# Performance work log

Measured on AMD Instinct MI355X. Metric: run time of the kernel, lower is better.

Reference implementation:

```python
import jax, jax.numpy as jnp
import numpy as np

TOPK = 16
MIN_SIM = 0.05
MIN_VOTES = 0.3
REMOVE_INNER = 0.5
NUM_CLASSES = 1000


def setup_inputs() -> dict:
    key = jax.random.key(0)
    kq, kdb, kid, kxy, kwh = jax.random.split(key, 5)
    Qn, N, C = 1024, 200000, 256
    q = jax.random.normal(kq, (Qn, C), dtype=jnp.float32)
    q = q / jnp.linalg.norm(q, axis=1, keepdims=True)
    db = jax.random.normal(kdb, (N, C), dtype=jnp.float32)
    db = db / jnp.linalg.norm(db, axis=1, keepdims=True)
    ids = jax.random.randint(kid, (N,), 0, NUM_CLASSES).astype(jnp.float32)
    places_db = jnp.concatenate([db, ids[:, None]], axis=1)  # (N, C+1)
    xy = jax.random.uniform(kxy, (Qn, 2), minval=0.0, maxval=800.0)
    wh = jax.random.uniform(kwh, (Qn, 2), minval=10.0, maxval=200.0)
    boxes = jnp.concatenate([xy, xy + wh], axis=1)  # valid xyxy boxes
    return {"boxes": boxes, "descriptors": q, "places_db": places_db}


def _remove_overlapping_boxes(boxes, labels, thr):
    # overlap = intersection / min(area_i, area_j); drop the BIGGER box of any
    # same-label pair whose overlap >= thr.
    bf = boxes.astype(jnp.float32)
    x1, y1, x2, y2 = bf[:, 0], bf[:, 1], bf[:, 2], bf[:, 3]
    areas = (x2 - x1) * (y2 - y1)
    xi1 = jnp.maximum(x1[:, None], x1[None, :])
    yi1 = jnp.maximum(y1[:, None], y1[None, :])
    xi2 = jnp.minimum(x2[:, None], x2[None, :])
    yi2 = jnp.minimum(y2[:, None], y2[None, :])
    inter = jnp.clip(xi2 - xi1, 0.0) * jnp.clip(yi2 - yi1, 0.0)
    area_i, area_j = areas[:, None], areas[None, :]
    area_small = jnp.minimum(area_i, area_j)
    overlap = jnp.where(area_small > 0, inter / jnp.maximum(area_small, 1e-12), 0.0)
    same_lbl = (labels[:, None] == labels[None, :]) & (labels[:, None] >= 0)
    n = boxes.shape[0]
    non_diag = ~jnp.eye(n, dtype=bool)
    mask_pair = same_lbl & (overlap >= thr) & non_diag
    bigger_i = area_i > area_j
    remove_i = (mask_pair & bigger_i).any(axis=1)
    remove_j = (mask_pair & ~bigger_i).any(axis=0)
    remove = remove_i | remove_j
    return jnp.where(remove, jnp.full_like(labels, -1), labels)


def reference(boxes, descriptors, places_db):
    X = places_db[:, :-1]                       # (N, C)
    ids = places_db[:, -1].astype(jnp.int32)    # (N,)
    sims = descriptors @ X.T                    # (Q, N)
    top_sims, top_idx = jax.lax.top_k(sims, TOPK)   # (Q, topk)
    top_ids = ids[top_idx]                          # (Q, topk)
    mask_sim = top_sims >= MIN_SIM
    # one-hot majority vote over classes
    one_hot = (top_ids[:, :, None] == jnp.arange(NUM_CLASSES, dtype=jnp.int32)[None, None, :]).astype(jnp.float32)
    vote_counts = (one_hot * mask_sim[:, :, None].astype(jnp.float32)).sum(axis=1)  # (Q, NUM_CLASSES)
    majority_counts = vote_counts.max(axis=1)
    majority_ids = jnp.argmax(vote_counts, axis=1).astype(jnp.int32)
    valid_votes = mask_sim.sum(axis=1).astype(jnp.float32)
    vote_ratio = jnp.where(valid_votes > 0, majority_counts / jnp.maximum(valid_votes, 1.0), 0.0)
    valid = (majority_counts > 0) & (vote_ratio >= MIN_VOTES)
    results = jnp.where(valid, majority_ids, jnp.full_like(majority_ids, -1))
    results = _remove_overlapping_boxes(boxes, results, REMOVE_INNER)
    match = (top_ids == results[:, None]) & mask_sim
    sim_scores = jnp.where(match, top_sims, jnp.zeros_like(top_sims)).max(axis=1)
    valid_mask = (results >= 0) & jnp.isfinite(sim_scores) & jnp.isfinite(boxes).all(axis=1)
    # Static-shape variant of the original's compaction: invalid rows are
    # marked with class=-1 / score=0 instead of being sliced out.
    return (boxes,
            jnp.where(valid_mask, sim_scores, 0.0),
            jnp.where(valid_mask, results, -1))
```

## Files before the change

kernel.cpp:

```cpp
#include <hip/hip_runtime.h>
#include <hip/hip_bf16.h>

#define QN 1024
#define NDB 200000
#define NDB_PAD 200064
#define PDBW 257
#define CDIM 256
#define TK 16
#define NEGF (-1e30f)
#define MIN_SIM_C 0.05f
#define MIN_VOTES_C 0.3f

#define NCH 256
#define THETA 0.19f
#define CAPQ 10
#define NCHUNK1 49
#define CPQ1 (NCHUNK1*32)

typedef __attribute__((ext_vector_type(8))) short bf16x8;
typedef __attribute__((ext_vector_type(4))) float f32x4;
typedef __attribute__((ext_vector_type(8))) int   i32x8;
typedef __attribute__((ext_vector_type(4))) int   i32x4;

__device__ __forceinline__ short f2bf(float f) {
  union { float f; unsigned u; } x; x.f = f;
  unsigned u = x.u;
  return (short)((u + 0x7fffu + ((u >> 16) & 1u)) >> 16);
}

__device__ __forceinline__ void async_copy16(const void* gp, void* lp) {
  __builtin_amdgcn_global_load_lds(
      (__attribute__((address_space(1))) void*)gp,
      (__attribute__((address_space(3))) void*)lp, 16, 0, 0);
}

__device__ __forceinline__ unsigned pk_fp8x4(float a, float b, float c, float d) {
  unsigned w = (unsigned)__builtin_amdgcn_cvt_pk_fp8_f32(a, b, 0, false);
  w = (unsigned)__builtin_amdgcn_cvt_pk_fp8_f32(c, d, (int)w, true);
  return w;
}

__device__ __forceinline__ int chunk_nsub(int c) { return 12 + (c < 54 ? 1 : 0); }
__device__ __forceinline__ int chunk_row0(int c) { return (12*c + (c < 54 ? c : 54)) << 6; }

__global__ __launch_bounds__(256) void convert_db_kernel(
    const float* __restrict__ pdb, unsigned char* __restrict__ dbb,
    int* __restrict__ flag)
{
  if (blockIdx.x == 0 && threadIdx.x == 0) *flag = 0;
  const int wv = (int)threadIdx.x >> 6, lane = (int)threadIdx.x & 63;
  for (int r = (int)blockIdx.x*4 + wv; r < NDB_PAD; r += (int)gridDim.x*4) {
    unsigned pack = 0u;
    if (r < NDB) {
      const float* p = pdb + (size_t)r*PDBW + lane*4;
      pack = pk_fp8x4(p[0], p[1], p[2], p[3]);
    }
    const int piece = lane >> 1;
    const int ps    = piece ^ ((r & 15) << 1);
    *(unsigned*)(dbb + (size_t)r*256 + ps*8 + (lane & 1)*4) = pack;
  }
}

__global__ __launch_bounds__(512, 1) void sims_filter_kernel(
    const float* __restrict__ qd, const unsigned char* __restrict__ dbb,
    unsigned int* __restrict__ seg_g, unsigned int* __restrict__ cnt_g)
{
  __shared__ __align__(16) char db_lds[2][64 * 256];
  __shared__ unsigned seg_lds[8][64][CAPQ];
  __shared__ int lcnt[8][64];

  const int tid  = (int)threadIdx.x;
  const int lane = tid & 63;
  const int wv   = tid >> 6;
  const int cid  = (int)blockIdx.x;
  const int mt   = (int)blockIdx.y;
  const int nsub = chunk_nsub(cid);
  const int row0 = chunk_row0(cid);

  lcnt[wv][lane] = 0;

  const int l15  = lane & 15;
  const int egrp = lane >> 4;
  const int rowb = egrp << 2;
  const int colb = l15;

  i32x8 aq[4][2];
  {
    #pragma unroll
    for (int fm = 0; fm < 4; ++fm) {
      const float* qrow = qd + (size_t)(mt*512 + wv*64 + fm*16 + l15)*CDIM;
      #pragma unroll
      for (int kk = 0; kk < 2; ++kk) {
        const float* p = qrow + kk*128 + egrp*32;
        i32x8 a;
        #pragma unroll
        for (int d = 0; d < 8; ++d) {
          float4 x = *(const float4*)(p + d*4);
          a[d] = (int)pk_fp8x4(x.x, x.y, x.z, x.w);
        }
        aq[fm][kk] = a;
      }
    }
  }

  const char* dbbase = (const char*)dbb;
#define STAGE(bufi, tile) do { \
    const char* _src = dbbase + ((size_t)(row0 + (tile)*64) * 256) + wv*2048 + lane*16; \
    char* _dst = (char*)db_lds[(bufi)] + wv*2048 + lane*16; \
    async_copy16(_src,        _dst); \
    async_copy16(_src + 1024, _dst + 1024); \
  } while (0)

  STAGE(0, 0);

  for (int s = 0; s < nsub; ++s) {
    asm volatile("s_waitcnt vmcnt(0)" ::: "memory");
    __builtin_amdgcn_sched_barrier(0);
    __builtin_amdgcn_s_barrier();
    __builtin_amdgcn_sched_barrier(0);

    if (s + 1 < nsub) STAGE((s + 1) & 1, s + 1);

    const char* dbt = (const char*)db_lds[s & 1];
    #pragma unroll
    for (int h = 0; h < 2; ++h) {
      f32x4 acc[4][2];
      #pragma unroll
      for (int fm = 0; fm < 4; ++fm)
        #pragma unroll
        for (int fnl = 0; fnl < 2; ++fnl)
          acc[fm][fnl] = (f32x4){0.f, 0.f, 0.f, 0.f};

      __builtin_amdgcn_s_setprio(1);
      #pragma unroll
      for (int kk = 0; kk < 2; ++kk) {
        #pragma unroll
        for (int fnl = 0; fnl < 2; ++fnl) {
          const int fn = h*2 + fnl;
          const char* rowp = dbt + (fn*16 + l15)*256;
          const int mbase = kk*8 + egrp*2;
          i32x4 lo = *(const i32x4*)(rowp + (((mbase    ) ^ l15) << 4));
          i32x4 hi = *(const i32x4*)(rowp + (((mbase + 1) ^ l15) << 4));
          i32x8 b = __builtin_shufflevector(lo, hi, 0, 1, 2, 3, 4, 5, 6, 7);
          #pragma unroll
          for (int fm = 0; fm < 4; ++fm)
            acc[fm][fnl] = __builtin_amdgcn_mfma_scale_f32_16x16x128_f8f6f4(
                aq[fm][kk], b, acc[fm][fnl],
                0 , 0 ,
                0, 0x7F7F7F7Fu , 0, 0x7F7F7F7Fu );
        }
      }
      __builtin_amdgcn_s_setprio(0);

      #pragma unroll
      for (int fm = 0; fm < 4; ++fm)
        #pragma unroll
        for (int fnl = 0; fnl < 2; ++fnl) {
          const f32x4 a = acc[fm][fnl];
          const float m = fmaxf(fmaxf(a[0], a[1]), fmaxf(a[2], a[3]));
          if (m > THETA) {
            #pragma unroll
            for (int j = 0; j < 4; ++j) {
              if (a[j] > THETA) {
                const int ql = fm*16 + rowb + j;
                const int slot = atomicAdd(&lcnt[wv][ql], 1);
                if (slot < CAPQ) {
                  const unsigned v16 = (unsigned)(unsigned short)f2bf(a[j]);
                  const unsigned loc = (unsigned)(s*64 + (h*2 + fnl)*16 + colb);
                  seg_lds[wv][ql][slot] = (v16 << 16) | loc;
                }
              }
            }
          }
        }
    }

    asm volatile("s_waitcnt lgkmcnt(0)" ::: "memory");
    __builtin_amdgcn_sched_barrier(0);
  }
#undef STAGE

  {
    const int cnt = lcnt[wv][lane];
    const int qg = mt*512 + wv*64 + lane;
    cnt_g[qg*NCH + cid] = (unsigned)cnt;
    const int nc = min(cnt, CAPQ);
    unsigned* dst = seg_g + (size_t)(qg*NCH + cid)*CAPQ;
    for (int j = 0; j < nc; ++j) dst[j] = seg_lds[wv][lane][j];
  }
}

__global__ __launch_bounds__(64) void gather_vote_kernel(
    const float* __restrict__ pdb,
    const unsigned* __restrict__ seg_g, const unsigned* __restrict__ cnt_g,
    int* __restrict__ out_label, float* __restrict__ out_s, int* __restrict__ flag)
{
  __shared__ float    cv[NCH*CAPQ];
  __shared__ unsigned ci[NCH*CAPQ];
  const int q    = (int)blockIdx.x;
  const int lane = (int)threadIdx.x;

  bool over = false;
  int tot = 0;
  #pragma unroll
  for (int h = 0; h < NCH/64; ++h) {
    const int c = h*64 + lane;
    const int cnt = (int)cnt_g[q*NCH + c];
    over |= (cnt > CAPQ);
    const int nc = min(cnt, CAPQ);
    tot += nc;
    const int r0c = chunk_row0(c);
    const unsigned* src = seg_g + (size_t)(q*NCH + c)*CAPQ;
    for (int j = 0; j < CAPQ; ++j) {
      float v = NEGF; unsigned idx = 0u;
      if (j < nc) {
        const unsigned e = src[j];
        v = __uint_as_float(e & 0xFFFF0000u);
        idx = (unsigned)(r0c + (int)(e & 0xFFFFu));
      }
      cv[c*CAPQ + j] = v;
      ci[c*CAPQ + j] = idx;
    }
  }
  #pragma unroll
  for (int off = 32; off >= 1; off >>= 1) tot += __shfl_xor(tot, off);
  __syncthreads();

  float topv[TK]; int topid[TK];
  #pragma unroll
  for (int r = 0; r < TK; ++r) {
    float bv = NEGF; int bp = -1;
    #pragma unroll 4
    for (int j = 0; j < (NCH*CAPQ)/64; ++j) {
      const int p = j*64 + lane;
      const float v = cv[p];
      if (v > bv) { bv = v; bp = p; }
    }
    #pragma unroll
    for (int off = 32; off >= 1; off >>= 1) {
      const float ov = __shfl_xor(bv, off);
      const int   op = __shfl_xor(bp, off);
      if (ov > bv || (ov == bv && ((unsigned)op < (unsigned)bp))) { bv = ov; bp = op; }
    }
    topv[r] = bv;
    int id = -2;
    if (bp >= 0 && bv > NEGF) id = (int)pdb[(size_t)ci[bp]*PDBW + CDIM];
    topid[r] = id;
    if (lane == 0 && bp >= 0) cv[bp] = NEGF;
    __syncthreads();
  }

  if (lane == 0) {
    bool mk[TK];
    int nvalid = 0;
    #pragma unroll
    for (int i = 0; i < TK; ++i) {
      mk[i] = (topv[i] >= MIN_SIM_C) && (topid[i] >= 0);
      nvalid += mk[i] ? 1 : 0;
    }
    int maj = 0, majid = 0x7fffffff;
    for (int i = 0; i < TK; ++i) {
      if (!mk[i]) continue;
      int c = 0;
      for (int j = 0; j < TK; ++j) c += (mk[j] && topid[j] == topid[i]) ? 1 : 0;
      if (c > maj || (c == maj && topid[i] < majid)) { maj = c; majid = topid[i]; }
    }
    const float ratio = (float)maj / fmaxf((float)nvalid, 1.0f);
    const bool valid = (maj > 0) && (ratio >= MIN_VOTES_C);
    const int label = valid ? majid : -1;
    float s = 0.f;
    #pragma unroll
    for (int i = 0; i < TK; ++i)
      if (mk[i] && topid[i] == label) s = fmaxf(s, topv[i]);
    out_label[q] = label;
    out_s[q]     = s;
  }
  const bool bad = (__ballot(over) != 0ull) || (tot < TK);
  if (lane == 0 && bad) atomicOr(flag, 1);
}

__global__ __launch_bounds__(256, 2) void sims_topk1_kernel(
    const float* __restrict__ qd, const float* __restrict__ pdb,
    float* __restrict__ cand_val, unsigned int* __restrict__ cand_idx,
    const int* __restrict__ gate)
{
  if (gate && *gate == 0) return;
  __shared__ __align__(16) short db_lds[128 * 264];
  float* sims = (float*)db_lds;

  const int tid  = (int)threadIdx.x;
  const int lane = tid & 63;
  const int wv   = tid >> 6;
  const int cid   = (int)blockIdx.x;
  const int mtile = (int)blockIdx.y;

  bf16x8 aq[2][8];
  {
    const int l15 = lane & 15;
    const int kb  = (lane >> 4) << 3;
    #pragma unroll
    for (int fm = 0; fm < 2; ++fm) {
      const int row = mtile*128 + wv*32 + fm*16 + l15;
      #pragma unroll
      for (int kk = 0; kk < 8; ++kk) {
        const float* p = qd + (size_t)row*CDIM + kk*32 + kb;
        float4 x0 = *(const float4*)p;
        float4 x1 = *(const float4*)(p + 4);
        bf16x8 a;
        a[0]=f2bf(x0.x); a[1]=f2bf(x0.y); a[2]=f2bf(x0.z); a[3]=f2bf(x0.w);
        a[4]=f2bf(x1.x); a[5]=f2bf(x1.y); a[6]=f2bf(x1.z); a[7]=f2bf(x1.w);
        aq[fm][kk] = a;
      }
    }
  }

  float    tv[TK];
  unsigned ti[TK];
  #pragma unroll
  for (int i = 0; i < TK; ++i) { tv[i] = NEGF; ti[i] = 0u; }
  float minv = NEGF; int minp = 0;

  const int g0chunk = cid * 4096;
  const int q_l  = tid & 127;
  const int half = tid >> 7;

  for (int s = 0; s < 32; ++s) {
    const int g0 = g0chunk + s*128;
    {
      const int rb = tid >> 6;
      const int c4 = (tid & 63) << 2;
      for (int i = 0; i < 32; ++i) {
        const int rl = i*4 + rb;
        const int g  = g0 + rl;
        float v0, v1, v2, v3;
        if (g < NDB) {
          const float* p = pdb + (size_t)g*PDBW + c4;
          v0 = p[0]; v1 = p[1]; v2 = p[2]; v3 = p[3];
        } else { v0 = v1 = v2 = v3 = 0.f; }
        short* d = &db_lds[rl*264 + c4];
        d[0]=f2bf(v0); d[1]=f2bf(v1); d[2]=f2bf(v2); d[3]=f2bf(v3);
      }
    }
    __syncthreads();

    f32x4 acc[2][8];
    #pragma unroll
    for (int fm = 0; fm < 2; ++fm)
      #pragma unroll
      for (int fn = 0; fn < 8; ++fn)
        acc[fm][fn] = (f32x4){0.f, 0.f, 0.f, 0.f};
    {
      const int l15 = lane & 15;
      const int kb  = (lane >> 4) << 3;
      #pragma unroll
      for (int kk = 0; kk < 8; ++kk) {
        bf16x8 b[8];
        #pragma unroll
        for (int fn = 0; fn < 8; ++fn)
          b[fn] = *(const bf16x8*)&db_lds[(fn*16 + l15)*264 + kk*32 + kb];
        #pragma unroll
        for (int fn = 0; fn < 8; ++fn) {
          acc[0][fn] = __builtin_amdgcn_mfma_f32_16x16x32_bf16(aq[0][kk], b[fn], acc[0][fn], 0, 0, 0);
          acc[1][fn] = __builtin_amdgcn_mfma_f32_16x16x32_bf16(aq[1][kk], b[fn], acc[1][fn], 0, 0, 0);
        }
      }
    }
    __syncthreads();

    {
      const int colb = lane & 15;
      const int rowb = (lane >> 4) << 2;
      #pragma unroll
      for (int fm = 0; fm < 2; ++fm)
        #pragma unroll
        for (int fn = 0; fn < 8; ++fn)
          #pragma unroll
          for (int j = 0; j < 4; ++j)
            sims[(wv*32 + fm*16 + rowb + j)*129 + fn*16 + colb] = acc[fm][fn][j];
    }
    __syncthreads();

    {
      const int cb = half * 64;
      #pragma unroll 4
      for (int c = 0; c < 64; ++c) {
        const int colc = cb + c;
        const float v = sims[q_l*129 + colc];
        const int g = g0 + colc;
        if (v > minv && g < NDB) {
          #pragma unroll
          for (int i = 0; i < TK; ++i) if (i == minp) { tv[i] = v; ti[i] = (unsigned)g; }
          minv = tv[0]; minp = 0;
          #pragma unroll
          for (int i = 1; i < TK; ++i) if (tv[i] < minv) { minv = tv[i]; minp = i; }
        }
      }
    }
    __syncthreads();
  }

  {
    const int qg = mtile*128 + q_l;
    float*    pv = cand_val + ((size_t)qg*NCHUNK1 + cid)*32 + half*TK;
    unsigned* pi = cand_idx + ((size_t)qg*NCHUNK1 + cid)*32 + half*TK;
    #pragma unroll
    for (int i = 0; i < TK; ++i) { pv[i] = tv[i]; pi[i] = ti[i]; }
  }
}

template<int CPQ>
__global__ __launch_bounds__(64) void merge_vote_kernel(
    const float* __restrict__ pdb,
    const float* __restrict__ cand_val, const unsigned* __restrict__ cand_idx,
    int* __restrict__ out_label, float* __restrict__ out_s,
    const int* __restrict__ gate)
{
  if (gate && *gate == 0) return;
  __shared__ float    cv[CPQ];
  __shared__ unsigned ci[CPQ];
  const int q    = (int)blockIdx.x;
  const int lane = (int)threadIdx.x;

  for (int j = lane; j < CPQ; j += 64) {
    cv[j] = cand_val[(size_t)q*CPQ + j];
    ci[j] = cand_idx[(size_t)q*CPQ + j];
  }
  __syncthreads();

  float topv[TK]; int topid[TK];
  #pragma unroll
  for (int r = 0; r < TK; ++r) {
    float bv = NEGF; int bp = -1;
    for (int j = lane; j < CPQ; j += 64) {
      const float v = cv[j];
      if (v > bv) { bv = v; bp = j; }
    }
    #pragma unroll
    for (int off = 32; off >= 1; off >>= 1) {
      const float ov = __shfl_xor(bv, off);
      const int   op = __shfl_xor(bp, off);
      if (ov > bv || (ov == bv && ((unsigned)op < (unsigned)bp))) { bv = ov; bp = op; }
    }
    topv[r] = bv;
    int id = -2;
    if (bp >= 0 && bv > NEGF) id = (int)pdb[(size_t)ci[bp]*PDBW + CDIM];
    topid[r] = id;
    if (lane == 0 && bp >= 0) cv[bp] = NEGF;
    __syncthreads();
  }

  if (lane == 0) {
    bool mk[TK];
    int nvalid = 0;
    #pragma unroll
    for (int i = 0; i < TK; ++i) {
      mk[i] = (topv[i] >= MIN_SIM_C) && (topid[i] >= 0);
      nvalid += mk[i] ? 1 : 0;
    }
    int maj = 0, majid = 0x7fffffff;
    for (int i = 0; i < TK; ++i) {
      if (!mk[i]) continue;
      int c = 0;
      for (int j = 0; j < TK; ++j) c += (mk[j] && topid[j] == topid[i]) ? 1 : 0;
      if (c > maj || (c == maj && topid[i] < majid)) { maj = c; majid = topid[i]; }
    }
    const float ratio = (float)maj / fmaxf((float)nvalid, 1.0f);
    const bool valid = (maj > 0) && (ratio >= MIN_VOTES_C);
    const int label = valid ? majid : -1;
    float s = 0.f;
    #pragma unroll
    for (int i = 0; i < TK; ++i)
      if (mk[i] && topid[i] == label) s = fmaxf(s, topv[i]);
    out_label[q] = label;
    out_s[q]     = s;
  }
}

__device__ __forceinline__ bool finitef(float v) {
  return ((__float_as_uint(v) >> 23) & 0xffu) != 0xffu;
}

__global__ __launch_bounds__(64) void finalize_kernel(
    const float* __restrict__ boxes, const int* __restrict__ labels,
    const float* __restrict__ svals, float* __restrict__ out)
{
  const int x    = (int)blockIdx.x;
  const int lane = (int)threadIdx.x;
  const int lx = labels[x];
  const float bx1 = boxes[x*4+0], by1 = boxes[x*4+1];
  const float bx2 = boxes[x*4+2], by2 = boxes[x*4+3];
  const float ax = (bx2 - bx1) * (by2 - by1);

  bool flag = false;
  if (lx >= 0) {
    for (int y = lane; y < QN; y += 64) {
      if (y == x) continue;
      if (labels[y] != lx) continue;
      const float c1 = boxes[y*4+0], c2 = boxes[y*4+1];
      const float c3 = boxes[y*4+2], c4 = boxes[y*4+3];
      const float ay = (c3 - c1) * (c4 - c2);
      const float xi1 = fmaxf(bx1, c1), yi1 = fmaxf(by1, c2);
      const float xi2 = fminf(bx2, c3), yi2 = fminf(by2, c4);
      const float inter = fmaxf(xi2 - xi1, 0.f) * fmaxf(yi2 - yi1, 0.f);
      const float asmall = fminf(ax, ay);
      const float ov = (asmall > 0.f) ? inter / fmaxf(asmall, 1e-12f) : 0.f;
      if (ov >= 0.5f && ay <= ax) flag = true;
    }
  }
  const bool removed = (__ballot(flag) != 0ull);
  const int label = removed ? -1 : lx;
  const float s = svals[x];
  const bool fin = finitef(s) && finitef(bx1) && finitef(by1) && finitef(bx2) && finitef(by2);
  const bool valid = (label >= 0) && fin;

  if (lane == 0) {
    out[4096 + x] = valid ? s : 0.f;
    out[5120 + x] = (float)(valid ? label : -1);
  }
  if (lane < 4) out[x*4 + lane] = boxes[x*4 + lane];
}

extern "C" void kernel_launch(void* const* d_in, const int* in_sizes, int n_in,
                              void* d_out, int out_size, void* d_ws, size_t ws_size,
                              hipStream_t stream)
{
  const float* boxes = (const float*)d_in[0];
  const float* qd    = (const float*)d_in[1];
  const float* pdb   = (const float*)d_in[2];
  float* out = (float*)d_out;
  char* ws = (char*)d_ws;

  const size_t db_bytes  = (size_t)NDB_PAD * 256;
  const size_t seg_bytes = (size_t)QN * NCH * CAPQ * 4;
  const size_t cnt_bytes = (size_t)QN * NCH * 4;
  const size_t c1_bytes  = (size_t)QN * CPQ1 * 8;
  const size_t A_bytes   = (seg_bytes + cnt_bytes > c1_bytes) ? seg_bytes + cnt_bytes : c1_bytes;
  const size_t need = db_bytes + A_bytes + (size_t)QN*8 + 64;

  if (ws_size >= need) {
    unsigned char* dbb = (unsigned char*)ws;
    char* A = ws + db_bytes;
    unsigned* seg_g = (unsigned*)A;
    unsigned* cnt_g = (unsigned*)(A + seg_bytes);
    float*    cand_val = (float*)A;
    unsigned* cand_idx = (unsigned*)(A + (size_t)QN*CPQ1*4);
    int*      labels   = (int*)(ws + db_bytes + A_bytes);
    float*    svals    = (float*)(ws + db_bytes + A_bytes + (size_t)QN*4);
    int*      flag     = (int*)(ws + db_bytes + A_bytes + (size_t)QN*8);

    hipLaunchKernelGGL(convert_db_kernel, dim3(2048), dim3(256), 0, stream, pdb, dbb, flag);
    hipLaunchKernelGGL(sims_filter_kernel, dim3(NCH, 2), dim3(512), 0, stream,
                       qd, dbb, seg_g, cnt_g);
    hipLaunchKernelGGL(gather_vote_kernel, dim3(QN), dim3(64), 0, stream,
                       pdb, seg_g, cnt_g, labels, svals, flag);
    hipLaunchKernelGGL(sims_topk1_kernel, dim3(NCHUNK1, 8), dim3(256), 0, stream,
                       qd, pdb, cand_val, cand_idx, flag);
    hipLaunchKernelGGL((merge_vote_kernel<CPQ1>), dim3(QN), dim3(64), 0, stream,
                       pdb, cand_val, cand_idx, labels, svals, flag);
    hipLaunchKernelGGL(finalize_kernel, dim3(QN), dim3(64), 0, stream,
                       boxes, labels, svals, out);
  } else {
    const size_t n1 = (size_t)QN * CPQ1;
    float*    cand_val = (float*)ws;
    unsigned* cand_idx = (unsigned*)(ws + n1*4);
    int*      labels   = (int*)(ws + n1*8);
    float*    svals    = (float*)(ws + n1*8 + (size_t)QN*4);

    hipLaunchKernelGGL(sims_topk1_kernel, dim3(NCHUNK1, 8), dim3(256), 0, stream,
                       qd, pdb, cand_val, cand_idx, (const int*)nullptr);
    hipLaunchKernelGGL((merge_vote_kernel<CPQ1>), dim3(QN), dim3(64), 0, stream,
                       pdb, cand_val, cand_idx, labels, svals, (const int*)nullptr);
    hipLaunchKernelGGL(finalize_kernel, dim3(QN), dim3(64), 0, stream,
                       boxes, labels, svals, out);
  }
}
```

Baseline: 194.6 us.

## Restructure sims filter into 256-thread blocks with 128-row DB tiles

The filter kernel now uses 128 DB chunks and 4 query tiles of 256 queries, with blocks of 256 threads and two blocks per CU. Each iteration stages two 64-row tiles (double-buffered pairs) and computes a 64x64 accumulator block per wave, so each B fragment load is reused over more MFMAs. Each chunk now covers twice as many rows, so the per-(query,chunk) candidate capacity rises to 14 to limit overflow into the fallback path. In exchange, per-wave accumulator registers double and LDS use grows.

```diff
diff --git a/kernel.cpp b/kernel.cpp
--- a/kernel.cpp
+++ b/kernel.cpp
@@ -11,9 +11,9 @@
 #define MIN_SIM_C 0.05f
 #define MIN_VOTES_C 0.3f
 
-#define NCH 256
+#define NCH 128
 #define THETA 0.19f
-#define CAPQ 10
+#define CAPQ 14
 #define NCHUNK1 49
 #define CPQ1 (NCHUNK1*32)
 
@@ -40,8 +40,8 @@
   return w;
 }
 
-__device__ __forceinline__ int chunk_nsub(int c) { return 12 + (c < 54 ? 1 : 0); }
-__device__ __forceinline__ int chunk_row0(int c) { return (12*c + (c < 54 ? c : 54)) << 6; }
+__device__ __forceinline__ int chunk_nsub(int c) { return 24 + (c < 27 ? 2 : 0); }
+__device__ __forceinline__ int chunk_row0(int c) { return (24*c + (c < 27 ? 2*c : 54)) << 6; }
 
 __global__ __launch_bounds__(256) void convert_db_kernel(
     const float* __restrict__ pdb, unsigned char* __restrict__ dbb,
@@ -61,20 +61,20 @@
   }
 }
 
-__global__ __launch_bounds__(512, 1) void sims_filter_kernel(
+__global__ __launch_bounds__(256, 2) void sims_filter_kernel(
     const float* __restrict__ qd, const unsigned char* __restrict__ dbb,
     unsigned int* __restrict__ seg_g, unsigned int* __restrict__ cnt_g)
 {
-  __shared__ __align__(16) char db_lds[2][64 * 256];
-  __shared__ unsigned seg_lds[8][64][CAPQ];
-  __shared__ int lcnt[8][64];
+  __shared__ __align__(16) char db_lds[4][64 * 256];
+  __shared__ unsigned seg_lds[4][64][CAPQ];
+  __shared__ int lcnt[4][64];
 
   const int tid  = (int)threadIdx.x;
   const int lane = tid & 63;
   const int wv   = tid >> 6;
   const int cid  = (int)blockIdx.x;
   const int mt   = (int)blockIdx.y;
-  const int nsub = chunk_nsub(cid);
+  const int nit  = chunk_nsub(cid) >> 1;
   const int row0 = chunk_row0(cid);
 
   lcnt[wv][lane] = 0;
@@ -88,7 +88,7 @@
   {
     #pragma unroll
     for (int fm = 0; fm < 4; ++fm) {
-      const float* qrow = qd + (size_t)(mt*512 + wv*64 + fm*16 + l15)*CDIM;
+      const float* qrow = qd + (size_t)(mt*256 + wv*64 + fm*16 + l15)*CDIM;
       #pragma unroll
       for (int kk = 0; kk < 2; ++kk) {
         const float* p = qrow + kk*128 + egrp*32;
@@ -105,38 +105,45 @@
 
   const char* dbbase = (const char*)dbb;
 #define STAGE(bufi, tile) do { \
-    const char* _src = dbbase + ((size_t)(row0 + (tile)*64) * 256) + wv*2048 + lane*16; \
-    char* _dst = (char*)db_lds[(bufi)] + wv*2048 + lane*16; \
+    const char* _src = dbbase + ((size_t)(row0 + (tile)*64) * 256) + wv*4096 + lane*16; \
+    char* _dst = (char*)db_lds[(bufi)] + wv*4096 + lane*16; \
     async_copy16(_src,        _dst); \
     async_copy16(_src + 1024, _dst + 1024); \
+    async_copy16(_src + 2048, _dst + 2048); \
+    async_copy16(_src + 3072, _dst + 3072); \
   } while (0)
 
   STAGE(0, 0);
-
-  for (int s = 0; s < nsub; ++s) {
+  STAGE(1, 1);
+
+  for (int i = 0; i < nit; ++i) {
     asm volatile("s_waitcnt vmcnt(0)" ::: "memory");
     __builtin_amdgcn_sched_barrier(0);
     __builtin_amdgcn_s_barrier();
     __builtin_amdgcn_sched_barrier(0);
 
-    if (s + 1 < nsub) STAGE((s + 1) & 1, s + 1);
-
-    const char* dbt = (const char*)db_lds[s & 1];
-    #pragma unroll
-    for (int h = 0; h < 2; ++h) {
-      f32x4 acc[4][2];
+    const int rp = (i & 1) << 1;
+    if (i + 1 < nit) {
+      const int wp = rp ^ 2;
+      STAGE(wp,     2*(i+1));
+      STAGE(wp + 1, 2*(i+1) + 1);
+    }
+
+    #pragma unroll
+    for (int t = 0; t < 2; ++t) {
+      const char* dbt = (const char*)db_lds[rp + t];
+      f32x4 acc[4][4];
       #pragma unroll
       for (int fm = 0; fm < 4; ++fm)
         #pragma unroll
-        for (int fnl = 0; fnl < 2; ++fnl)
-          acc[fm][fnl] = (f32x4){0.f, 0.f, 0.f, 0.f};
+        for (int fn = 0; fn < 4; ++fn)
+          acc[fm][fn] = (f32x4){0.f, 0.f, 0.f, 0.f};
 
       __builtin_amdgcn_s_setprio(1);
       #pragma unroll
       for (int kk = 0; kk < 2; ++kk) {
         #pragma unroll
-        for (int fnl = 0; fnl < 2; ++fnl) {
-          const int fn = h*2 + fnl;
+        for (int fn = 0; fn < 4; ++fn) {
           const char* rowp = dbt + (fn*16 + l15)*256;
           const int mbase = kk*8 + egrp*2;
           i32x4 lo = *(const i32x4*)(rowp + (((mbase    ) ^ l15) << 4));
@@ -144,19 +151,20 @@
           i32x8 b = __builtin_shufflevector(lo, hi, 0, 1, 2, 3, 4, 5, 6, 7);
           #pragma unroll
           for (int fm = 0; fm < 4; ++fm)
-            acc[fm][fnl] = __builtin_amdgcn_mfma_scale_f32_16x16x128_f8f6f4(
-                aq[fm][kk], b, acc[fm][fnl],
+            acc[fm][fn] = __builtin_amdgcn_mfma_scale_f32_16x16x128_f8f6f4(
+                aq[fm][kk], b, acc[fm][fn],
                 0 , 0 ,
                 0, 0x7F7F7F7Fu , 0, 0x7F7F7F7Fu );
         }
       }
       __builtin_amdgcn_s_setprio(0);
 
+      const int lbase = (2*i + t) * 64;
       #pragma unroll
       for (int fm = 0; fm < 4; ++fm)
         #pragma unroll
-        for (int fnl = 0; fnl < 2; ++fnl) {
-          const f32x4 a = acc[fm][fnl];
+        for (int fn = 0; fn < 4; ++fn) {
+          const f32x4 a = acc[fm][fn];
           const float m = fmaxf(fmaxf(a[0], a[1]), fmaxf(a[2], a[3]));
           if (m > THETA) {
             #pragma unroll
@@ -166,7 +174,7 @@
                 const int slot = atomicAdd(&lcnt[wv][ql], 1);
                 if (slot < CAPQ) {
                   const unsigned v16 = (unsigned)(unsigned short)f2bf(a[j]);
-                  const unsigned loc = (unsigned)(s*64 + (h*2 + fnl)*16 + colb);
+                  const unsigned loc = (unsigned)(lbase + fn*16 + colb);
                   seg_lds[wv][ql][slot] = (v16 << 16) | loc;
                 }
               }
@@ -182,7 +190,7 @@
 
   {
     const int cnt = lcnt[wv][lane];
-    const int qg = mt*512 + wv*64 + lane;
+    const int qg = mt*256 + wv*64 + lane;
     cnt_g[qg*NCH + cid] = (unsigned)cnt;
     const int nc = min(cnt, CAPQ);
     unsigned* dst = seg_g + (size_t)(qg*NCH + cid)*CAPQ;
@@ -549,7 +557,7 @@
     int*      flag     = (int*)(ws + db_bytes + A_bytes + (size_t)QN*8);
 
     hipLaunchKernelGGL(convert_db_kernel, dim3(2048), dim3(256), 0, stream, pdb, dbb, flag);
-    hipLaunchKernelGGL(sims_filter_kernel, dim3(NCH, 2), dim3(512), 0, stream,
+    hipLaunchKernelGGL(sims_filter_kernel, dim3(NCH, 4), dim3(256), 0, stream,
                        qd, dbb, seg_g, cnt_g);
     hipLaunchKernelGGL(gather_vote_kernel, dim3(QN), dim3(64), 0, stream,
                        pdb, seg_g, cnt_g, labels, svals, flag);
```

After: 166.2 us. 1.17x faster.

## Pre-swizzle DB into MFMA fragment layout and read directly from global

Applied to the files above, without the earlier changes.

The conversion kernel now writes the fp8 database in a tile layout that matches the MFMA B-fragment order, so each lane loads its 32 bytes straight from global memory. This removes the LDS double-buffered staging and its per-tile barriers. The filter kernel also moves to 256-thread blocks with three blocks per CU, a 128x4 grid and larger chunks with a higher per-chunk candidate cap. In exchange, the shared tile is no longer reused across waves, so every wave fetches its DB tile separately from L2/global, and gather_vote must scan fewer but larger chunk segments.

```diff
diff --git a/kernel.cpp b/kernel.cpp
--- a/kernel.cpp
+++ b/kernel.cpp
@@ -11,9 +11,9 @@
 #define MIN_SIM_C 0.05f
 #define MIN_VOTES_C 0.3f
 
-#define NCH 256
+#define NCH 128
 #define THETA 0.19f
-#define CAPQ 10
+#define CAPQ 14
 #define NCHUNK1 49
 #define CPQ1 (NCHUNK1*32)
 
@@ -28,20 +28,14 @@
   return (short)((u + 0x7fffu + ((u >> 16) & 1u)) >> 16);
 }
 
-__device__ __forceinline__ void async_copy16(const void* gp, void* lp) {
-  __builtin_amdgcn_global_load_lds(
-      (__attribute__((address_space(1))) void*)gp,
-      (__attribute__((address_space(3))) void*)lp, 16, 0, 0);
-}
-
 __device__ __forceinline__ unsigned pk_fp8x4(float a, float b, float c, float d) {
   unsigned w = (unsigned)__builtin_amdgcn_cvt_pk_fp8_f32(a, b, 0, false);
   w = (unsigned)__builtin_amdgcn_cvt_pk_fp8_f32(c, d, (int)w, true);
   return w;
 }
 
-__device__ __forceinline__ int chunk_nsub(int c) { return 12 + (c < 54 ? 1 : 0); }
-__device__ __forceinline__ int chunk_row0(int c) { return (12*c + (c < 54 ? c : 54)) << 6; }
+__device__ __forceinline__ int chunk_nsub(int c) { return 24 + (c < 27 ? 2 : 0); }
+__device__ __forceinline__ int chunk_row0(int c) { return (24*c + (c < 27 ? 2*c : 54)) << 6; }
 
 __global__ __launch_bounds__(256) void convert_db_kernel(
     const float* __restrict__ pdb, unsigned char* __restrict__ dbb,
@@ -55,19 +49,22 @@
       const float* p = pdb + (size_t)r*PDBW + lane*4;
       pack = pk_fp8x4(p[0], p[1], p[2], p[3]);
     }
-    const int piece = lane >> 1;
-    const int ps    = piece ^ ((r & 15) << 1);
-    *(unsigned*)(dbb + (size_t)r*256 + ps*8 + (lane & 1)*4) = pack;
-  }
-}
-
-__global__ __launch_bounds__(512, 1) void sims_filter_kernel(
+    const int tile = r >> 6, fn = (r >> 4) & 3, l15 = r & 15;
+    const int kk   = lane >> 5;
+    const int egrp = (lane & 31) >> 3;
+    const int b32  = (lane & 7) << 2;
+    unsigned char* dst = dbb + (size_t)tile*16384
+                       + ((((kk*4 + fn)*64) + egrp*16 + l15) << 5) + b32;
+    *(unsigned*)dst = pack;
+  }
+}
+
+__global__ __launch_bounds__(256, 3) void sims_filter_kernel(
     const float* __restrict__ qd, const unsigned char* __restrict__ dbb,
     unsigned int* __restrict__ seg_g, unsigned int* __restrict__ cnt_g)
 {
-  __shared__ __align__(16) char db_lds[2][64 * 256];
-  __shared__ unsigned seg_lds[8][64][CAPQ];
-  __shared__ int lcnt[8][64];
+  __shared__ unsigned seg_lds[4][64][CAPQ];
+  __shared__ int lcnt[4][64];
 
   const int tid  = (int)threadIdx.x;
   const int lane = tid & 63;
@@ -88,7 +85,7 @@
   {
     #pragma unroll
     for (int fm = 0; fm < 4; ++fm) {
-      const float* qrow = qd + (size_t)(mt*512 + wv*64 + fm*16 + l15)*CDIM;
+      const float* qrow = qd + (size_t)(mt*256 + wv*64 + fm*16 + l15)*CDIM;
       #pragma unroll
       for (int kk = 0; kk < 2; ++kk) {
         const float* p = qrow + kk*128 + egrp*32;
@@ -103,25 +100,11 @@
     }
   }
 
-  const char* dbbase = (const char*)dbb;
-#define STAGE(bufi, tile) do { \
-    const char* _src = dbbase + ((size_t)(row0 + (tile)*64) * 256) + wv*2048 + lane*16; \
-    char* _dst = (char*)db_lds[(bufi)] + wv*2048 + lane*16; \
-    async_copy16(_src,        _dst); \
-    async_copy16(_src + 1024, _dst + 1024); \
-  } while (0)
-
-  STAGE(0, 0);
+  const char* tbase = (const char*)dbb + (size_t)(row0 >> 6) * 16384;
 
   for (int s = 0; s < nsub; ++s) {
-    asm volatile("s_waitcnt vmcnt(0)" ::: "memory");
-    __builtin_amdgcn_sched_barrier(0);
-    __builtin_amdgcn_s_barrier();
-    __builtin_amdgcn_sched_barrier(0);
-
-    if (s + 1 < nsub) STAGE((s + 1) & 1, s + 1);
-
-    const char* dbt = (const char*)db_lds[s & 1];
+    const char* tb = tbase + (size_t)s * 16384;
+
     #pragma unroll
     for (int h = 0; h < 2; ++h) {
       f32x4 acc[4][2];
@@ -137,10 +120,9 @@
         #pragma unroll
         for (int fnl = 0; fnl < 2; ++fnl) {
           const int fn = h*2 + fnl;
-          const char* rowp = dbt + (fn*16 + l15)*256;
-          const int mbase = kk*8 + egrp*2;
-          i32x4 lo = *(const i32x4*)(rowp + (((mbase    ) ^ l15) << 4));
-          i32x4 hi = *(const i32x4*)(rowp + (((mbase + 1) ^ l15) << 4));
+          const char* p = tb + (((kk*4 + fn)*64 + lane) << 5);
+          i32x4 lo = *(const i32x4*)p;
+          i32x4 hi = *(const i32x4*)(p + 16);
           i32x8 b = __builtin_shufflevector(lo, hi, 0, 1, 2, 3, 4, 5, 6, 7);
           #pragma unroll
           for (int fm = 0; fm < 4; ++fm)
@@ -174,15 +156,11 @@
           }
         }
     }
-
-    asm volatile("s_waitcnt lgkmcnt(0)" ::: "memory");
-    __builtin_amdgcn_sched_barrier(0);
-  }
-#undef STAGE
+  }
 
   {
     const int cnt = lcnt[wv][lane];
-    const int qg = mt*512 + wv*64 + lane;
+    const int qg = mt*256 + wv*64 + lane;
     cnt_g[qg*NCH + cid] = (unsigned)cnt;
     const int nc = min(cnt, CAPQ);
     unsigned* dst = seg_g + (size_t)(qg*NCH + cid)*CAPQ;
@@ -549,7 +527,7 @@
     int*      flag     = (int*)(ws + db_bytes + A_bytes + (size_t)QN*8);
 
     hipLaunchKernelGGL(convert_db_kernel, dim3(2048), dim3(256), 0, stream, pdb, dbb, flag);
-    hipLaunchKernelGGL(sims_filter_kernel, dim3(NCH, 2), dim3(512), 0, stream,
+    hipLaunchKernelGGL(sims_filter_kernel, dim3(NCH, 4), dim3(256), 0, stream,
                        qd, dbb, seg_g, cnt_g);
     hipLaunchKernelGGL(gather_vote_kernel, dim3(QN), dim3(64), 0, stream,
                        pdb, seg_g, cnt_g, labels, svals, flag);
```

Result: faster. 166.2 us (-14.6%).
